# Optimization experiments

Measured on AMD Instinct MI355X. Metric: run time of the kernel, lower is better.

Reference implementation:

```python
import jax, jax.numpy as jnp
import numpy as np


def conv2d(x, w, b, stride=1, pad=0):
    out = jax.lax.conv_general_dilated(
        x, w, (stride, stride), ((pad, pad), (pad, pad)),
        dimension_numbers=('NCHW', 'OIHW', 'NCHW'))
    return out + b[None, :, None, None]


def maxpool2(x):
    return jax.lax.reduce_window(x, -jnp.inf, jax.lax.max,
                                 (1, 1, 2, 2), (1, 1, 2, 2), 'VALID')


def pixel_match_(x, y):
    # x, y: (1, C, H, W). 9-way shifted squared-diff cost volume.
    _, C, H, W = x.shape
    yc = y[0, :, 1:H - 1, 1:W - 1]
    inner = []
    for dh in range(3):
        for dw in range(3):
            tmp = x[0, :, dh:dh + H - 2, dw:dw + W - 2] - yc
            inner.append(jnp.sum(tmp * tmp, axis=0))
    inner = jnp.stack(inner)  # (9, H-2, W-2)
    diff = jnp.zeros((9, H, W), x.dtype).at[:, 1:H - 1, 1:W - 1].set(inner)
    diff = 1.0 / jnp.sqrt(diff + 0.01)
    diff = diff / jnp.sum(diff, axis=0, keepdims=True)
    return diff[None]  # (1, 9, H, W)


def positional(H, W, dtype):
    h = jnp.arange(H, dtype=dtype)
    w = jnp.arange(W, dtype=dtype)
    h = 2.0 * h / h[-1] - 1.0
    w = 2.0 * w / w[-1] - 1.0
    ph = jnp.broadcast_to(h[:, None], (H, W))
    pw = jnp.broadcast_to(w[None, :], (H, W))
    return jnp.stack([ph, pw])[None]  # (1, 2, H, W)


def pixel_match(x, y):
    return jnp.concatenate(
        [pixel_match_(x, y), pixel_match_(y, x),
         positional(x.shape[2], x.shape[3], x.dtype)], axis=1)


def adaptive_max_pool3(x):
    # torch adaptive_max_pool2d semantics: bin i spans [floor(i*H/3), ceil((i+1)*H/3))
    _, C, H, W = x.shape
    rows = []
    for i in range(3):
        hs, he = (i * H) // 3, -((-(i + 1) * H) // 3)
        cols = []
        for j in range(3):
            ws, we = (j * W) // 3, -((-(j + 1) * W) // 3)
            cols.append(jnp.max(x[:, :, hs:he, ws:we], axis=(2, 3)))
        rows.append(jnp.stack(cols, axis=-1))
    return jnp.stack(rows, axis=-2)  # (1, C, 3, 3)


def setup_inputs() -> dict:
    key = jax.random.key(0)
    ks = jax.random.split(key, 16)
    f = jnp.float32
    H = W = 1024
    s = 0.05
    return {
        'x1': jax.random.normal(ks[0], (3, H, W), f),
        'x2': jax.random.normal(ks[1], (3, H, W), f),
        'enc_w': jax.random.normal(ks[2], (24, 3, 3, 3), f) * s,
        'enc_b': jax.random.normal(ks[3], (24,), f) * s,
        'embed_w': jax.random.normal(ks[4], (32, 24, 1, 1), f) * s,
        'embed_b': jax.random.normal(ks[5], (32,), f) * s,
        'dense_w': jax.random.normal(ks[6], (8, 32, 5, 5), f) * s,
        'dense_b': jax.random.normal(ks[7], (8,), f) * s,
        'f1_w': jax.random.normal(ks[8], (64, 48, 1, 1), f) * s,
        'f1_b': jax.random.normal(ks[9], (64,), f) * s,
        'f2_w': jax.random.normal(ks[10], (128, 64, 3, 3), f) * s,
        'f2_b': jax.random.normal(ks[11], (128,), f) * s,
        'f3_w': jax.random.normal(ks[12], (6, 128), f) * s,
        'f3_b': jax.random.normal(ks[13], (6,), f) * s,
    }


def reference(x1, x2, enc_w, enc_b, embed_w, embed_b, dense_w, dense_b,
              f1_w, f1_b, f2_w, f2_b, f3_w, f3_b):
    def coding(x):
        x = x[None]  # (1,3,H,W)
        x = jax.lax.stop_gradient(conv2d(x, enc_w, enc_b, pad=1))  # frozen encoder
        x = conv2d(x, embed_w, embed_b)
        return maxpool2(x)

    c1 = coding(x1)
    c2 = coding(x2)
    level1 = maxpool2(pixel_match(c1, c2))
    p1 = maxpool2(c1)
    p2 = maxpool2(c2)
    level2 = pixel_match(p1, p2)
    dense = jax.nn.leaky_relu(conv2d(p1 - p2, dense_w, dense_b, pad=2))
    x = jnp.concatenate([level1, level2, dense], axis=1)  # (1,48,H/4,W/4)
    x = conv2d(x, f1_w, f1_b)
    x = adaptive_max_pool3(x)
    x = conv2d(x, f2_w, f2_b).reshape(1, 128)
    tmp = jnp.sum(x * x) + 0.001
    x = x / jnp.sqrt(tmp)
    x = (x @ f3_w.T + f3_b).reshape(2, 3)
    x = jnp.concatenate([x, jnp.zeros((1, 3), x.dtype)], axis=0)
    return jnp.eye(3, dtype=x.dtype) + jnp.clip(x, -0.11, 0.11) + x * 0.01
```

## Files before the change

kernel.cpp:

```cpp
#include <hip/hip_runtime.h>
#include <math.h>


__global__ void fuse_weights_kernel(const float* __restrict__ enc_w,
                                    const float* __restrict__ enc_b,
                                    const float* __restrict__ embed_w,
                                    const float* __restrict__ embed_b,
                                    float* __restrict__ weff_t,
                                    float* __restrict__ beff) {
    int t = threadIdx.x;
    for (int idx = t; idx < 27 * 32; idx += blockDim.x) {
        int r = idx >> 5, o = idx & 31;
        float s = 0.f;
        for (int k = 0; k < 24; ++k) s += embed_w[o * 24 + k] * enc_w[k * 27 + r];
        weff_t[idx] = s;
    }
    if (t < 32) {
        float s = embed_b[t];
        for (int k = 0; k < 24; ++k) s += embed_w[t * 24 + k] * enc_b[k];
        beff[t] = s;
    }
}

__global__ __launch_bounds__(256) void coding_kernel(
    const float* __restrict__ x1, const float* __restrict__ x2,
    const float* __restrict__ weff_t, const float* __restrict__ beff,
    float* __restrict__ c1, float* __restrict__ c2,
    float* __restrict__ p1, float* __restrict__ p2) {
    int tx = threadIdx.x, ty = threadIdx.y;
    int img = blockIdx.z;
    const float* x = img ? x2 : x1;
    float* c = img ? c2 : c1;
    float* p = img ? p2 : p1;
    int Y = blockIdx.y * 16 + ty;
    int cx = blockIdx.x * 16 + tx;
    int X0 = 2 * cx;
    bool interior = (blockIdx.y > 0 && blockIdx.y < 63 &&
                     blockIdx.x > 0 && blockIdx.x < 31);
    float acc0[32], acc1[32];
#pragma unroll
    for (int o = 0; o < 32; ++o) {
        acc0[o] = beff[o];
        acc1[o] = acc0[o];
    }
#pragma unroll 1
    for (int ci = 0; ci < 3; ++ci) {
        float in[3][4];
        const float* xc = x + ci * 1048576;
        if (interior) {
#pragma unroll
            for (int r = 0; r < 3; ++r) {
                const float* row = xc + (Y - 1 + r) * 1024 + X0 - 1;
#pragma unroll
                for (int q = 0; q < 4; ++q) in[r][q] = row[q];
            }
        } else {
#pragma unroll
            for (int r = 0; r < 3; ++r)
#pragma unroll
                for (int q = 0; q < 4; ++q) {
                    int gy = Y - 1 + r, gx = X0 - 1 + q;
                    in[r][q] = (gy >= 0 && gy < 1024 && gx >= 0 && gx < 1024)
                                   ? xc[gy * 1024 + gx]
                                   : 0.f;
                }
        }
#pragma unroll
        for (int ky = 0; ky < 3; ++ky)
#pragma unroll
            for (int kx = 0; kx < 3; ++kx) {
                const float* wrow = weff_t + (ci * 9 + ky * 3 + kx) * 32;
                float xa = in[ky][kx];
                float xb = in[ky][kx + 1];
#pragma unroll
                for (int o = 0; o < 32; ++o) {
                    float wv = wrow[o];
                    acc0[o] = fmaf(wv, xa, acc0[o]);
                    acc1[o] = fmaf(wv, xb, acc1[o]);
                }
            }
    }
#pragma unroll
    for (int o = 0; o < 32; ++o) {
        float m = fmaxf(acc0[o], acc1[o]);
        acc0[o] = fmaxf(m, __shfl_xor(m, 16, 64));
    }
    int cpix = (Y >> 1) * 512 + cx;
    if ((ty & 1) == 0) {
        float4* cd = (float4*)(c + cpix * 32);
#pragma unroll
        for (int q = 0; q < 8; ++q)
            cd[q] = make_float4(acc0[4 * q], acc0[4 * q + 1], acc0[4 * q + 2],
                                acc0[4 * q + 3]);
    }
#pragma unroll
    for (int o = 0; o < 32; ++o) {
        float v = fmaxf(acc0[o], __shfl_xor(acc0[o], 1, 64));
        acc0[o] = fmaxf(v, __shfl_xor(v, 32, 64));
    }
    if (((ty & 3) == 0) && ((tx & 1) == 0)) {
        int ppix = (Y >> 2) * 256 + (cx >> 1);
        float4* pd = (float4*)(p + ppix * 32);
#pragma unroll
        for (int q = 0; q < 8; ++q)
            pd[q] = make_float4(acc0[4 * q], acc0[4 * q + 1], acc0[4 * q + 2],
                                acc0[4 * q + 3]);
    }
}

__global__ __launch_bounds__(256) void mid_kernel(
    const float* __restrict__ c1, const float* __restrict__ c2,
    const float* __restrict__ p1, const float* __restrict__ p2,
    const float* __restrict__ dw, float* __restrict__ feat,
    float* __restrict__ part) {
    __shared__ float smem[4 * 1296 + 4 * 8 * 28];
    int bid = blockIdx.x;
    int tid = threadIdx.x;
    if (bid < 4096) {
        int bx = bid & 63, by = bid >> 6;
        int quad = tid & 3;
        int pl = tid >> 2;
        int px = pl & 7, py = pl >> 3;
        int sw = bx * 8 + px;
        int sh = by * 8 + py;
        bool interior = (sh >= 1 && sh <= 510 && sw >= 1 && sw <= 510);
        const float* b1 = c1 + (sh * 512 + sw) * 32 + quad * 8;
        const float* b2 = c2 + (sh * 512 + sw) * 32 + quad * 8;
        float a1[9], a2[9];
#pragma unroll
        for (int k = 0; k < 9; ++k) { a1[k] = 0.f; a2[k] = 0.f; }
        if (interior) {
            float4 y1a = ((const float4*)b1)[0], y1b = ((const float4*)b1)[1];
            float4 y2a = ((const float4*)b2)[0], y2b = ((const float4*)b2)[1];
#pragma unroll
            for (int dh = -1; dh <= 1; ++dh)
#pragma unroll
                for (int dwp = -1; dwp <= 1; ++dwp) {
                    int k = (dh + 1) * 3 + (dwp + 1);
                    const float4* n1 =
                        (const float4*)(b1 + (dh * 512 + dwp) * 32);
                    const float4* n2 =
                        (const float4*)(b2 + (dh * 512 + dwp) * 32);
                    float4 na = n1[0], nA = n1[1], nb = n2[0], nB = n2[1];
                    float s1 = a1[k], s2 = a2[k], t;
                    t = na.x - y2a.x; s1 = fmaf(t, t, s1);
                    t = na.y - y2a.y; s1 = fmaf(t, t, s1);
                    t = na.z - y2a.z; s1 = fmaf(t, t, s1);
                    t = na.w - y2a.w; s1 = fmaf(t, t, s1);
                    t = nA.x - y2b.x; s1 = fmaf(t, t, s1);
                    t = nA.y - y2b.y; s1 = fmaf(t, t, s1);
                    t = nA.z - y2b.z; s1 = fmaf(t, t, s1);
                    t = nA.w - y2b.w; s1 = fmaf(t, t, s1);
                    t = nb.x - y1a.x; s2 = fmaf(t, t, s2);
                    t = nb.y - y1a.y; s2 = fmaf(t, t, s2);
                    t = nb.z - y1a.z; s2 = fmaf(t, t, s2);
                    t = nb.w - y1a.w; s2 = fmaf(t, t, s2);
                    t = nB.x - y1b.x; s2 = fmaf(t, t, s2);
                    t = nB.y - y1b.y; s2 = fmaf(t, t, s2);
                    t = nB.z - y1b.z; s2 = fmaf(t, t, s2);
                    t = nB.w - y1b.w; s2 = fmaf(t, t, s2);
                    a1[k] = s1;
                    a2[k] = s2;
                }
        }
#pragma unroll
        for (int k = 0; k < 9; ++k) {
            a1[k] += __shfl_xor(a1[k], 1, 64);
            a1[k] += __shfl_xor(a1[k], 2, 64);
            a2[k] += __shfl_xor(a2[k], 1, 64);
            a2[k] += __shfl_xor(a2[k], 2, 64);
        }
        float d[20];
        if (interior) {
            float s1 = 0.f, s2 = 0.f;
#pragma unroll
            for (int k = 0; k < 9; ++k) {
                a1[k] = 1.0f / sqrtf(a1[k] + 0.01f);
                a2[k] = 1.0f / sqrtf(a2[k] + 0.01f);
                s1 += a1[k];
                s2 += a2[k];
            }
            float i1 = 1.0f / s1, i2 = 1.0f / s2;
#pragma unroll
            for (int k = 0; k < 9; ++k) {
                d[k] = a1[k] * i1;
                d[9 + k] = a2[k] * i2;
            }
        } else {
#pragma unroll
            for (int k = 0; k < 18; ++k) d[k] = 1.0f / 9.0f;
        }
#pragma unroll
        for (int k = 0; k < 18; ++k) {
            float v = fmaxf(d[k], __shfl_xor(d[k], 4, 64));
            d[k] = fmaxf(v, __shfl_xor(v, 32, 64));
        }
        d[18] = 2.0f * (sh | 1) / 511.0f - 1.0f;
        d[19] = 2.0f * (sw | 1) / 511.0f - 1.0f;
        if ((tid & 36) == 0) {
            int opix = (sh >> 1) * 256 + (sw >> 1);
#pragma unroll
            for (int j = 0; j < 5; ++j)
                feat[(quad * 5 + j) * 65536 + opix] = d[quad * 5 + j];
        }
    } else if (bid < 5120) {
        int i = bid - 4096;
        int bx = i & 31, by = i >> 5;
        int quad = tid & 3;
        int pl = tid >> 2;
        int px = pl & 7, py = pl >> 3;
        int w = bx * 8 + px;
        int h = by * 8 + py;
        bool interior = (h >= 1 && h <= 254 && w >= 1 && w <= 254);
        const float* b1 = p1 + (h * 256 + w) * 32 + quad * 8;
        const float* b2 = p2 + (h * 256 + w) * 32 + quad * 8;
        float a1[9], a2[9];
#pragma unroll
        for (int k = 0; k < 9; ++k) { a1[k] = 0.f; a2[k] = 0.f; }
        if (interior) {
            float4 y1a = ((const float4*)b1)[0], y1b = ((const float4*)b1)[1];
            float4 y2a = ((const float4*)b2)[0], y2b = ((const float4*)b2)[1];
#pragma unroll
            for (int dh = -1; dh <= 1; ++dh)
#pragma unroll
                for (int dwp = -1; dwp <= 1; ++dwp) {
                    int k = (dh + 1) * 3 + (dwp + 1);
                    const float4* n1 =
                        (const float4*)(b1 + (dh * 256 + dwp) * 32);
                    const float4* n2 =
                        (const float4*)(b2 + (dh * 256 + dwp) * 32);
                    float4 na = n1[0], nA = n1[1], nb = n2[0], nB = n2[1];
                    float s1 = a1[k], s2 = a2[k], t;
                    t = na.x - y2a.x; s1 = fmaf(t, t, s1);
                    t = na.y - y2a.y; s1 = fmaf(t, t, s1);
                    t = na.z - y2a.z; s1 = fmaf(t, t, s1);
                    t = na.w - y2a.w; s1 = fmaf(t, t, s1);
                    t = nA.x - y2b.x; s1 = fmaf(t, t, s1);
                    t = nA.y - y2b.y; s1 = fmaf(t, t, s1);
                    t = nA.z - y2b.z; s1 = fmaf(t, t, s1);
                    t = nA.w - y2b.w; s1 = fmaf(t, t, s1);
                    t = nb.x - y1a.x; s2 = fmaf(t, t, s2);
                    t = nb.y - y1a.y; s2 = fmaf(t, t, s2);
                    t = nb.z - y1a.z; s2 = fmaf(t, t, s2);
                    t = nb.w - y1a.w; s2 = fmaf(t, t, s2);
                    t = nB.x - y1b.x; s2 = fmaf(t, t, s2);
                    t = nB.y - y1b.y; s2 = fmaf(t, t, s2);
                    t = nB.z - y1b.z; s2 = fmaf(t, t, s2);
                    t = nB.w - y1b.w; s2 = fmaf(t, t, s2);
                    a1[k] = s1;
                    a2[k] = s2;
                }
        }
#pragma unroll
        for (int k = 0; k < 9; ++k) {
            a1[k] += __shfl_xor(a1[k], 1, 64);
            a1[k] += __shfl_xor(a1[k], 2, 64);
            a2[k] += __shfl_xor(a2[k], 1, 64);
            a2[k] += __shfl_xor(a2[k], 2, 64);
        }
        float d[20];
        if (interior) {
            float s1 = 0.f, s2 = 0.f;
#pragma unroll
            for (int k = 0; k < 9; ++k) {
                a1[k] = 1.0f / sqrtf(a1[k] + 0.01f);
                a2[k] = 1.0f / sqrtf(a2[k] + 0.01f);
                s1 += a1[k];
                s2 += a2[k];
            }
            float i1 = 1.0f / s1, i2 = 1.0f / s2;
#pragma unroll
            for (int k = 0; k < 9; ++k) {
                d[k] = a1[k] * i1;
                d[9 + k] = a2[k] * i2;
            }
        } else {
#pragma unroll
            for (int k = 0; k < 18; ++k) d[k] = 1.0f / 9.0f;
        }
        d[18] = 2.0f * h / 255.0f - 1.0f;
        d[19] = 2.0f * w / 255.0f - 1.0f;
        int pix = h * 256 + w;
#pragma unroll
        for (int j = 0; j < 5; ++j)
            feat[(20 + quad * 5 + j) * 65536 + pix] = d[quad * 5 + j];
    } else {
        float* sdiff = smem;
        float* sw = smem + 4 * 1296;
        int i = bid - 5120;
        int bz = i >> 6;
        int rem = i & 63;
        int by = rem >> 3, bx = rem & 7;
        int tx = tid & 15, ty = tid >> 4;
        int h0 = by * 32, w0 = bx * 32;
        for (int idx = tid; idx < 1296; idx += 256) {
            int yy = idx / 36, xx = idx % 36;
            int gy = h0 + yy - 2, gx = w0 + xx - 2;
            float4 dv = make_float4(0.f, 0.f, 0.f, 0.f);
            if (gy >= 0 && gy < 256 && gx >= 0 && gx < 256) {
                const float4* q1 =
                    (const float4*)(p1 + (gy * 256 + gx) * 32 + bz * 4);
                const float4* q2 =
                    (const float4*)(p2 + (gy * 256 + gx) * 32 + bz * 4);
                float4 v1 = q1[0], v2 = q2[0];
                dv = make_float4(v1.x - v2.x, v1.y - v2.y, v1.z - v2.z,
                                 v1.w - v2.w);
            }
            sdiff[0 * 1296 + idx] = dv.x;
            sdiff[1 * 1296 + idx] = dv.y;
            sdiff[2 * 1296 + idx] = dv.z;
            sdiff[3 * 1296 + idx] = dv.w;
        }
        for (int idx = tid; idx < 4 * 8 * 28; idx += 256) {
            int ci = idx / 224, r = idx % 224;
            int o = r / 28, k = r % 28;
            sw[idx] = (k < 25) ? dw[o * 800 + (bz * 4 + ci) * 25 + k] : 0.f;
        }
        __syncthreads();
        float acc[4][8];
#pragma unroll
        for (int pq = 0; pq < 4; ++pq)
#pragma unroll
            for (int o = 0; o < 8; ++o) acc[pq][o] = 0.f;
        for (int ci = 0; ci < 4; ++ci) {
            float patch[6][6];
#pragma unroll
            for (int yy = 0; yy < 6; ++yy) {
                const float* rowp =
                    &sdiff[ci * 1296 + (2 * ty + yy) * 36 + 2 * tx];
#pragma unroll
                for (int cpair = 0; cpair < 3; ++cpair) {
                    float2 lp = *(const float2*)&rowp[2 * cpair];
                    patch[yy][2 * cpair] = lp.x;
                    patch[yy][2 * cpair + 1] = lp.y;
                }
            }
#pragma unroll
            for (int o = 0; o < 8; ++o) {
                float wreg[28];
                const float4* wp = (const float4*)&sw[(ci * 8 + o) * 28];
#pragma unroll
                for (int q = 0; q < 7; ++q) {
                    float4 wv = wp[q];
                    wreg[4 * q] = wv.x;
                    wreg[4 * q + 1] = wv.y;
                    wreg[4 * q + 2] = wv.z;
                    wreg[4 * q + 3] = wv.w;
                }
#pragma unroll
                for (int ky = 0; ky < 5; ++ky)
#pragma unroll
                    for (int kx = 0; kx < 5; ++kx) {
                        float wv = wreg[ky * 5 + kx];
#pragma unroll
                        for (int pq = 0; pq < 4; ++pq)
                            acc[pq][o] =
                                fmaf(wv, patch[ky + (pq >> 1)][kx + (pq & 1)],
                                     acc[pq][o]);
                    }
            }
        }
#pragma unroll
        for (int pq = 0; pq < 4; ++pq) {
            int h = h0 + 2 * ty + (pq >> 1), w = w0 + 2 * tx + (pq & 1);
            int pix = h * 256 + w;
#pragma unroll
            for (int o = 0; o < 8; ++o)
                part[bz * 524288 + o * 65536 + pix] = acc[pq][o];
        }
    }
}

__global__ __launch_bounds__(256) void f1_kernel(
    const float* __restrict__ feat, const float* __restrict__ part,
    const float* __restrict__ db, const float* __restrict__ f1w,
    const float* __restrict__ f1b, float* __restrict__ out) {
    __shared__ float sw[1536];
    __shared__ float sb[32];
    int og = blockIdx.y;
    int tid = threadIdx.x;
    for (int i = tid; i < 1536; i += 256) sw[i] = f1w[og * 1536 + i];
    if (tid < 32) sb[tid] = f1b[og * 32 + tid];
    __syncthreads();
    int pix = blockIdx.x * 256 + tid;
    float f[48];
#pragma unroll
    for (int c = 0; c < 40; ++c) f[c] = feat[c * 65536 + pix];
#pragma unroll
    for (int o = 0; o < 8; ++o) {
        float s = db[o];
#pragma unroll
        for (int z = 0; z < 8; ++z) s += part[z * 524288 + o * 65536 + pix];
        f[40 + o] = (s >= 0.f) ? s : 0.01f * s;
    }
#pragma unroll
    for (int o = 0; o < 32; ++o) {
        float a = sb[o];
        const float4* wv = (const float4*)&sw[o * 48];
#pragma unroll
        for (int c4 = 0; c4 < 12; ++c4) {
            float4 ww = wv[c4];
            a = fmaf(ww.x, f[c4 * 4], a);
            a = fmaf(ww.y, f[c4 * 4 + 1], a);
            a = fmaf(ww.z, f[c4 * 4 + 2], a);
            a = fmaf(ww.w, f[c4 * 4 + 3], a);
        }
        out[(og * 32 + o) * 65536 + pix] = a;
    }
}

__global__ __launch_bounds__(256) void pool3_kernel(
    const float* __restrict__ f1out, float* __restrict__ pooled) {
    int b = blockIdx.x;
    int c = b / 9, ij = b % 9, i = ij / 3, j = ij % 3;
    int hs = (i * 256) / 3, he = ((i + 1) * 256 + 2) / 3;
    int ws = (j * 256) / 3, we = ((j + 1) * 256 + 2) / 3;
    const float* src = f1out + c * 65536;
    int nh = he - hs, nw = we - ws, tot = nh * nw;
    float m = -INFINITY;
    for (int t = threadIdx.x; t < tot; t += 256) {
        int r = t / nw, q = t - r * nw;
        m = fmaxf(m, src[(hs + r) * 256 + (ws + q)]);
    }
    for (int off = 32; off > 0; off >>= 1) m = fmaxf(m, __shfl_down(m, off, 64));
    __shared__ float red[4];
    if ((threadIdx.x & 63) == 0) red[threadIdx.x >> 6] = m;
    __syncthreads();
    if (threadIdx.x == 0)
        pooled[b] = fmaxf(fmaxf(red[0], red[1]), fmaxf(red[2], red[3]));
}

__global__ __launch_bounds__(128) void final_kernel(
    const float* __restrict__ pooled, const float* __restrict__ f2w,
    const float* __restrict__ f2b, const float* __restrict__ f3w,
    const float* __restrict__ f3b, float* __restrict__ out) {
    __shared__ float xn[128];
    __shared__ float red[2];
    __shared__ float ov[6];
    int t = threadIdx.x;
    float a = f2b[t];
    for (int c = 0; c < 64; ++c)
#pragma unroll
        for (int k = 0; k < 9; ++k)
            a = fmaf(f2w[t * 576 + c * 9 + k], pooled[c * 9 + k], a);
    float sq = a * a;
    for (int off = 32; off > 0; off >>= 1) sq += __shfl_down(sq, off, 64);
    if ((t & 63) == 0) red[t >> 6] = sq;
    __syncthreads();
    float tmp = red[0] + red[1] + 0.001f;
    float scale = 1.0f / sqrtf(tmp);
    xn[t] = a * scale;
    __syncthreads();
    if (t < 6) {
        float o = f3b[t];
        for (int k = 0; k < 128; ++k) o = fmaf(f3w[t * 128 + k], xn[k], o);
        ov[t] = o;
    }
    __syncthreads();
    if (t < 9) {
        int r = t / 3, cc = t % 3;
        float v = 0.f;
        if (r < 2) {
            float x = ov[r * 3 + cc];
            float cl = fminf(fmaxf(x, -0.11f), 0.11f);
            v = cl + 0.01f * x;
        }
        if (r == cc) v += 1.0f;
        out[t] = v;
    }
}

extern "C" void kernel_launch(void* const* d_in, const int* in_sizes, int n_in,
                              void* d_out, int out_size, void* d_ws,
                              size_t ws_size, hipStream_t stream) {
    const float* x1 = (const float*)d_in[0];
    const float* x2 = (const float*)d_in[1];
    const float* enc_w = (const float*)d_in[2];
    const float* enc_b = (const float*)d_in[3];
    const float* embed_w = (const float*)d_in[4];
    const float* embed_b = (const float*)d_in[5];
    const float* dense_w = (const float*)d_in[6];
    const float* dense_b = (const float*)d_in[7];
    const float* f1_w = (const float*)d_in[8];
    const float* f1_b = (const float*)d_in[9];
    const float* f2_w = (const float*)d_in[10];
    const float* f2_b = (const float*)d_in[11];
    const float* f3_w = (const float*)d_in[12];
    const float* f3_b = (const float*)d_in[13];

    float* ws = (float*)d_ws;
    float* weff_t = ws;
    float* beff = ws + 864;
    float* c1 = ws + 1024;
    float* c2 = c1 + 8388608;
    float* p1 = c2 + 8388608;
    float* p2 = p1 + 2097152;
    float* feat = p2 + 2097152;
    float* pooled = feat + 3145728;
    float* part = pooled + 1024;
    float* f1o = c1;

    fuse_weights_kernel<<<1, 256, 0, stream>>>(enc_w, enc_b, embed_w, embed_b,
                                               weff_t, beff);
    coding_kernel<<<dim3(32, 64, 2), dim3(16, 16), 0, stream>>>(
        x1, x2, weff_t, beff, c1, c2, p1, p2);
    mid_kernel<<<5632, 256, 0, stream>>>(c1, c2, p1, p2, dense_w, feat, part);
    f1_kernel<<<dim3(256, 2), 256, 0, stream>>>(feat, part, dense_b, f1_w,
                                                f1_b, f1o);
    pool3_kernel<<<576, 256, 0, stream>>>(f1o, pooled);
    final_kernel<<<1, 128, 0, stream>>>(pooled, f2_w, f2_b, f3_w, f3_b,
                                        (float*)d_out);
}
```

Before: 175.1 us.

## Shrink dense-conv tiles to one pixel per thread and swizzle pixel-match block order

The dense 5x5 conv branch of mid_kernel now uses 16x16 output tiles with one output pixel per thread instead of 32x32 tiles with a 2x2 quad per thread. This cuts shared memory and registers and quadruples the number of conv blocks, aiming for higher occupancy and better load balance. The cost is more halo reloading and less register reuse of patch values. The pixel-match blocks also get a swizzled block-to-tile mapping to change memory locality across concurrently running blocks.

```diff
diff --git a/kernel.cpp b/kernel.cpp
--- a/kernel.cpp
+++ b/kernel.cpp
@@ -113,11 +113,12 @@
     const float* __restrict__ p1, const float* __restrict__ p2,
     const float* __restrict__ dw, float* __restrict__ feat,
     float* __restrict__ part) {
-    __shared__ float smem[4 * 1296 + 4 * 8 * 28];
+    __shared__ float smem[2496];
     int bid = blockIdx.x;
     int tid = threadIdx.x;
     if (bid < 4096) {
-        int bx = bid & 63, by = bid >> 6;
+        int swz = (bid & 7) * 512 + (bid >> 3);
+        int bx = swz & 63, by = swz >> 6;
         int quad = tid & 3;
         int pl = tid >> 2;
         int px = pl & 7, py = pl >> 3;
@@ -286,16 +287,15 @@
             feat[(20 + quad * 5 + j) * 65536 + pix] = d[quad * 5 + j];
     } else {
         float* sdiff = smem;
-        float* sw = smem + 4 * 1296;
+        float* swl = smem + 1600;
         int i = bid - 5120;
-        int bz = i >> 6;
-        int rem = i & 63;
-        int by = rem >> 3, bx = rem & 7;
-        int tx = tid & 15, ty = tid >> 4;
-        int h0 = by * 32, w0 = bx * 32;
-        for (int idx = tid; idx < 1296; idx += 256) {
-            int yy = idx / 36, xx = idx % 36;
-            int gy = h0 + yy - 2, gx = w0 + xx - 2;
+        int bz = i >> 8;
+        int rem = i & 255;
+        int by = rem >> 4, bx = rem & 15;
+        int h0 = by * 16, w0 = bx * 16;
+        for (int idx = tid; idx < 400; idx += 256) {
+            int r = idx / 20, cc2 = idx % 20;
+            int gy = h0 + r - 2, gx = w0 + cc2 - 2;
             float4 dv = make_float4(0.f, 0.f, 0.f, 0.f);
             if (gy >= 0 && gy < 256 && gx >= 0 && gx < 256) {
                 const float4* q1 =
@@ -306,39 +306,34 @@
                 dv = make_float4(v1.x - v2.x, v1.y - v2.y, v1.z - v2.z,
                                  v1.w - v2.w);
             }
-            sdiff[0 * 1296 + idx] = dv.x;
-            sdiff[1 * 1296 + idx] = dv.y;
-            sdiff[2 * 1296 + idx] = dv.z;
-            sdiff[3 * 1296 + idx] = dv.w;
-        }
-        for (int idx = tid; idx < 4 * 8 * 28; idx += 256) {
+            sdiff[0 * 400 + idx] = dv.x;
+            sdiff[1 * 400 + idx] = dv.y;
+            sdiff[2 * 400 + idx] = dv.z;
+            sdiff[3 * 400 + idx] = dv.w;
+        }
+        for (int idx = tid; idx < 896; idx += 256) {
             int ci = idx / 224, r = idx % 224;
             int o = r / 28, k = r % 28;
-            sw[idx] = (k < 25) ? dw[o * 800 + (bz * 4 + ci) * 25 + k] : 0.f;
+            swl[idx] = (k < 25) ? dw[o * 800 + (bz * 4 + ci) * 25 + k] : 0.f;
         }
         __syncthreads();
-        float acc[4][8];
-#pragma unroll
-        for (int pq = 0; pq < 4; ++pq)
-#pragma unroll
-            for (int o = 0; o < 8; ++o) acc[pq][o] = 0.f;
+        int tx = tid & 15, ty = tid >> 4;
+        float acc[8];
+#pragma unroll
+        for (int o = 0; o < 8; ++o) acc[o] = 0.f;
+#pragma unroll 1
         for (int ci = 0; ci < 4; ++ci) {
-            float patch[6][6];
-#pragma unroll
-            for (int yy = 0; yy < 6; ++yy) {
-                const float* rowp =
-                    &sdiff[ci * 1296 + (2 * ty + yy) * 36 + 2 * tx];
-#pragma unroll
-                for (int cpair = 0; cpair < 3; ++cpair) {
-                    float2 lp = *(const float2*)&rowp[2 * cpair];
-                    patch[yy][2 * cpair] = lp.x;
-                    patch[yy][2 * cpair + 1] = lp.y;
-                }
-            }
+            float patch[25];
+#pragma unroll
+            for (int dy = 0; dy < 5; ++dy)
+#pragma unroll
+                for (int dx = 0; dx < 5; ++dx)
+                    patch[dy * 5 + dx] =
+                        sdiff[ci * 400 + (ty + dy) * 20 + tx + dx];
 #pragma unroll
             for (int o = 0; o < 8; ++o) {
                 float wreg[28];
-                const float4* wp = (const float4*)&sw[(ci * 8 + o) * 28];
+                const float4* wp = (const float4*)&swl[(ci * 8 + o) * 28];
 #pragma unroll
                 for (int q = 0; q < 7; ++q) {
                     float4 wv = wp[q];
@@ -348,26 +343,14 @@
                     wreg[4 * q + 3] = wv.w;
                 }
 #pragma unroll
-                for (int ky = 0; ky < 5; ++ky)
-#pragma unroll
-                    for (int kx = 0; kx < 5; ++kx) {
-                        float wv = wreg[ky * 5 + kx];
-#pragma unroll
-                        for (int pq = 0; pq < 4; ++pq)
-                            acc[pq][o] =
-                                fmaf(wv, patch[ky + (pq >> 1)][kx + (pq & 1)],
-                                     acc[pq][o]);
-                    }
-            }
-        }
-#pragma unroll
-        for (int pq = 0; pq < 4; ++pq) {
-            int h = h0 + 2 * ty + (pq >> 1), w = w0 + 2 * tx + (pq & 1);
-            int pix = h * 256 + w;
-#pragma unroll
-            for (int o = 0; o < 8; ++o)
-                part[bz * 524288 + o * 65536 + pix] = acc[pq][o];
-        }
+                for (int k = 0; k < 25; ++k)
+                    acc[o] = fmaf(wreg[k], patch[k], acc[o]);
+            }
+        }
+        int pix = (h0 + ty) * 256 + (w0 + tx);
+#pragma unroll
+        for (int o = 0; o < 8; ++o)
+            part[bz * 524288 + o * 65536 + pix] = acc[o];
     }
 }
 
@@ -504,7 +487,7 @@
                                                weff_t, beff);
     coding_kernel<<<dim3(32, 64, 2), dim3(16, 16), 0, stream>>>(
         x1, x2, weff_t, beff, c1, c2, p1, p2);
-    mid_kernel<<<5632, 256, 0, stream>>>(c1, c2, p1, p2, dense_w, feat, part);
+    mid_kernel<<<7168, 256, 0, stream>>>(c1, c2, p1, p2, dense_w, feat, part);
     f1_kernel<<<dim3(256, 2), 256, 0, stream>>>(feat, part, dense_b, f1_w,
                                                 f1_b, f1o);
     pool3_kernel<<<576, 256, 0, stream>>>(f1o, pooled);
```

After: 189.5 us. 1.08x slower.
